# Kernel optimization log

Hardware: AMD Instinct MI355X
Metric: run time of the kernel (lower is better)

## Reference

```python
import jax, jax.numpy as jnp
import numpy as np

B, S, E, D, H = 32, 4096, 512, 512, 512


def setup_inputs() -> dict:
    key = jax.random.key(0)
    ks = jax.random.split(key, 7)
    scale = 1.0 / np.sqrt(H)
    return {
        "encoder_hiddens": jax.random.normal(ks[0], (B, S, E), dtype=jnp.float32),
        "decoder_hidden": jax.random.normal(ks[1], (B, D), dtype=jnp.float32),
        "W_enc": jax.random.uniform(ks[2], (H, E), jnp.float32, -scale, scale),
        "b_enc": jax.random.uniform(ks[3], (H,), jnp.float32, -scale, scale),
        "W_dec": jax.random.uniform(ks[4], (H, D), jnp.float32, -scale, scale),
        "b_dec": jax.random.uniform(ks[5], (H,), jnp.float32, -scale, scale),
        "v": jax.random.uniform(ks[6], (H,), jnp.float32, -scale, scale),
    }


def reference(encoder_hiddens, decoder_hidden, W_enc, b_enc, W_dec, b_dec, v):
    # Projections (the two small GEMMs of the original per-timestep loop, batched)
    enc_hs = jnp.einsum("bse,he->bsh", encoder_hiddens, W_enc) + b_enc  # [B,S,H]
    dec_h = decoder_hidden @ W_dec.T + b_dec                            # [B,H]

    # Ragged-length detection: the torch loop breaks at the first all-zero
    # projected encoder row; positions at/after that are excluded (cumulative AND).
    nonzero = jnp.any(enc_hs != 0, axis=-1)                             # [B,S]
    valid = jnp.cumprod(nonzero.astype(jnp.int32), axis=1).astype(bool)

    # Additive (Bahdanau) scores: v . tanh(enc_hs + dec_h)
    scores = jnp.einsum("h,bsh->bs", v, jnp.tanh(enc_hs + dec_h[:, None, :]))
    scores = jnp.where(valid, scores, -jnp.inf)
    attn = jax.nn.softmax(scores, axis=1)                               # [B,S]
    attn = jnp.where(valid, attn, 0.0)

    # Weighted sum of encoder states -> context vector [B,1,E]
    return jnp.sum(encoder_hiddens * attn[..., None], axis=1, keepdims=True)
```

## Files before the change

### kernel.cpp

```cpp
#include <hip/hip_runtime.h>
#include <hip/hip_bf16.h>

#define BATCH 32
#define SEQ   4096
#define EDIM  512
#define HDIM  512
#define NCHUNK 64
#define NBLK  (BATCH * NCHUNK)

typedef unsigned short u16;
typedef unsigned int   u32;

typedef __bf16 bf16x8 __attribute__((ext_vector_type(8)));
typedef float  f32x4  __attribute__((ext_vector_type(4)));

__device__ __forceinline__ u16 bf_rne(float x) {
    u32 u = __float_as_uint(x);
    u32 r = (u + 0x7fffu + ((u >> 16) & 1u)) >> 16;
    return (u16)r;
}
__device__ __forceinline__ u32 pack2(u16 lo, u16 hi) {
    return (u32)lo | ((u32)hi << 16);
}
__device__ __forceinline__ float tanh_fast(float x) {
    float e = __builtin_amdgcn_exp2f(x * 2.88539008177793f);
    return 1.0f - 2.0f * __builtin_amdgcn_rcpf(e + 1.0f);
}

__global__ void prep_kernel(const float* __restrict__ W_enc, uint4* __restrict__ wpack,
                            const float* __restrict__ dec, const float* __restrict__ Wd,
                            const float* __restrict__ b_enc, const float* __restrict__ b_dec,
                            float* __restrict__ dec_bias) {
    int bid = blockIdx.x;
    int t = threadIdx.x;
    if (bid < 4096) {
        int wave = t >> 6, lane = t & 63;
        int p = bid * 4 + wave;
        int b = p >> 9, h = p & 511;
        const float4* wr = reinterpret_cast<const float4*>(Wd)  + h * 128;
        const float4* dr = reinterpret_cast<const float4*>(dec) + b * 128;
        float4 w0 = wr[lane * 2], w1 = wr[lane * 2 + 1];
        float4 d0 = dr[lane * 2], d1 = dr[lane * 2 + 1];
        float s = w0.x * d0.x + w0.y * d0.y + w0.z * d0.z + w0.w * d0.w
                + w1.x * d1.x + w1.y * d1.y + w1.z * d1.z + w1.w * d1.w;
#pragma unroll
        for (int m = 1; m < 64; m <<= 1) s += __shfl_xor(s, m, 64);
        if (lane == 0) dec_bias[p] = s + b_dec[h] + b_enc[h];
    } else {
        int id   = (bid - 4096) * 256 + t;
        int nsub = id >> 10;
        int rem  = id & 1023;
        int kc   = rem >> 6;
        int lane = rem & 63;
        int row  = nsub * 16 + (lane & 15);
        int col  = kc * 32 + (lane >> 4) * 8;
        const float* src = W_enc + row * EDIM + col;
        uint4 o;
        o.x = pack2(bf_rne(src[0]), bf_rne(src[1]));
        o.y = pack2(bf_rne(src[2]), bf_rne(src[3]));
        o.z = pack2(bf_rne(src[4]), bf_rne(src[5]));
        o.w = pack2(bf_rne(src[6]), bf_rne(src[7]));
        wpack[id] = o;
    }
}

__global__ __launch_bounds__(256, 2) void fused_kernel(
    const float* __restrict__ X, const uint4* __restrict__ Wp,
    const float* __restrict__ bias, const float* __restrict__ v,
    float* __restrict__ cpart, float* __restrict__ mpart, float* __restrict__ lpart)
{
    __shared__ alignas(16) u16 Abuf[2][64 * 72];
    __shared__ float sred[4][64];
    __shared__ float pbuf[64];

    const int tid  = threadIdx.x;
    const int wave = tid >> 6, lane = tid & 63;
    const int quad = lane >> 4, l15 = lane & 15;
    const int blk  = blockIdx.x;
    const int b    = blk >> 6;
    const long row0 = (long)blk * 64;
    const float4* X4 = reinterpret_cast<const float4*>(X + row0 * EDIM);

    f32x4 acc[4][8] = {};

    const int r  = tid >> 2;
    const int c8 = tid & 3;

    float4 pA = X4[r * 128 + c8 * 2];
    float4 pB = X4[r * 128 + c8 * 2 + 1];
    {
        uint4 w;
        w.x = pack2(bf_rne(pA.x), bf_rne(pA.y));
        w.y = pack2(bf_rne(pA.z), bf_rne(pA.w));
        w.z = pack2(bf_rne(pB.x), bf_rne(pB.y));
        w.w = pack2(bf_rne(pB.z), bf_rne(pB.w));
        *reinterpret_cast<uint4*>(&Abuf[0][r * 72 + c8 * 8]) = w;
    }
    pA = X4[r * 128 + 8 + c8 * 2];
    pB = X4[r * 128 + 8 + c8 * 2 + 1];
    __syncthreads();

    for (int ch = 0; ch < 16; ch++) {
        const u16* Ab = Abuf[ch & 1];

        uint4 braw[8];
#pragma unroll
        for (int jj = 0; jj < 8; jj++)
            braw[jj] = Wp[((wave * 8 + jj) * 16 + ch) * 64 + lane];

        float4 nA, nB;
        if (ch < 14) {
            nA = X4[r * 128 + (ch + 2) * 8 + c8 * 2];
            nB = X4[r * 128 + (ch + 2) * 8 + c8 * 2 + 1];
        }

        bf16x8 af[4];
#pragma unroll
        for (int i = 0; i < 4; i++)
            af[i] = *reinterpret_cast<const bf16x8*>(&Ab[(i * 16 + l15) * 72 + quad * 8]);
#pragma unroll
        for (int jj = 0; jj < 8; jj++) {
            bf16x8 bfr = __builtin_bit_cast(bf16x8, braw[jj]);
#pragma unroll
            for (int i = 0; i < 4; i++)
                acc[i][jj] = __builtin_amdgcn_mfma_f32_16x16x32_bf16(
                    af[i], bfr, acc[i][jj], 0, 0, 0);
        }

        if (ch < 15) {
            uint4 w;
            w.x = pack2(bf_rne(pA.x), bf_rne(pA.y));
            w.y = pack2(bf_rne(pA.z), bf_rne(pA.w));
            w.z = pack2(bf_rne(pB.x), bf_rne(pB.y));
            w.w = pack2(bf_rne(pB.z), bf_rne(pB.w));
            *reinterpret_cast<uint4*>(&Abuf[(ch & 1) ^ 1][r * 72 + c8 * 8]) = w;
        }
        __syncthreads();
        if (ch < 14) { pA = nA; pB = nB; }
    }

    float hb[8], hv[8];
#pragma unroll
    for (int jj = 0; jj < 8; jj++) {
        int h = wave * 128 + jj * 16 + l15;
        hb[jj] = bias[b * HDIM + h];
        hv[jj] = v[h];
    }
    float s_acc[16];
#pragma unroll
    for (int x = 0; x < 16; x++) s_acc[x] = 0.f;
#pragma unroll
    for (int i = 0; i < 4; i++)
#pragma unroll
        for (int jj = 0; jj < 8; jj++)
#pragma unroll
            for (int rr = 0; rr < 4; rr++)
                s_acc[i * 4 + rr] += hv[jj] * tanh_fast(acc[i][jj][rr] + hb[jj]);

#pragma unroll
    for (int m = 1; m < 16; m <<= 1)
#pragma unroll
        for (int x = 0; x < 16; x++)
            s_acc[x] += __shfl_xor(s_acc[x], m, 16);

    if (l15 == 0) {
#pragma unroll
        for (int x = 0; x < 16; x++) {
            int i = x >> 2, rr = x & 3;
            sred[wave][i * 16 + quad * 4 + rr] = s_acc[x];
        }
    }
    __syncthreads();

    if (tid < 64) {
        float sc = sred[0][tid] + sred[1][tid] + sred[2][tid] + sred[3][tid];
        float mx = sc;
#pragma unroll
        for (int m = 1; m < 64; m <<= 1) mx = fmaxf(mx, __shfl_xor(mx, m, 64));
        float p = __builtin_amdgcn_exp2f((sc - mx) * 1.44269504088896f);
        float l = p;
#pragma unroll
        for (int m = 1; m < 64; m <<= 1) l += __shfl_xor(l, m, 64);
        pbuf[tid] = p;
        if (tid == 0) { mpart[blk] = mx; lpart[blk] = l; }
    }
    __syncthreads();

    const float2* Xp = reinterpret_cast<const float2*>(X + row0 * EDIM) + tid;
    float ax0 = 0.f, ay0 = 0.f, ax1 = 0.f, ay1 = 0.f;
#pragma unroll 2
    for (int s = 0; s < 64; s += 8) {
        float2 x[8];
#pragma unroll
        for (int k = 0; k < 8; k++) x[k] = Xp[(s + k) * 256];
#pragma unroll
        for (int k = 0; k < 8; k += 2) {
            float w0 = pbuf[s + k], w1 = pbuf[s + k + 1];
            ax0 = fmaf(w0, x[k].x,     ax0);
            ay0 = fmaf(w0, x[k].y,     ay0);
            ax1 = fmaf(w1, x[k + 1].x, ax1);
            ay1 = fmaf(w1, x[k + 1].y, ay1);
        }
    }
    reinterpret_cast<float2*>(cpart)[blk * 256 + tid] =
        make_float2(ax0 + ax1, ay0 + ay1);
}

__global__ __launch_bounds__(256) void combine_k(const float* __restrict__ cpart,
                                                 const float* __restrict__ mpart,
                                                 const float* __restrict__ lpart,
                                                 float* __restrict__ out) {
    __shared__ float wbuf[64];
    __shared__ float linv_s;
    int b = blockIdx.x, t = threadIdx.x;
    if (t < 64) {
        float m = mpart[b * 64 + t];
        float M = m;
#pragma unroll
        for (int k = 1; k < 64; k <<= 1) M = fmaxf(M, __shfl_xor(M, k, 64));
        float w = __builtin_amdgcn_exp2f((m - M) * 1.44269504088896f);
        float lw = lpart[b * 64 + t] * w;
        float L = lw;
#pragma unroll
        for (int k = 1; k < 64; k <<= 1) L += __shfl_xor(L, k, 64);
        wbuf[t] = w;
        if (t == 0) linv_s = 1.0f / L;
    }
    __syncthreads();
    const float2* cp = reinterpret_cast<const float2*>(cpart) + (long)b * 64 * 256 + t;
    float ax = 0.f, ay = 0.f;
#pragma unroll 2
    for (int i = 0; i < 64; i += 8) {
        float2 x[8];
#pragma unroll
        for (int k = 0; k < 8; k++) x[k] = cp[(i + k) * 256];
#pragma unroll
        for (int k = 0; k < 8; k++) {
            float w = wbuf[i + k];
            ax = fmaf(w, x[k].x, ax);
            ay = fmaf(w, x[k].y, ay);
        }
    }
    float inv = linv_s;
    reinterpret_cast<float2*>(out)[b * 256 + t] = make_float2(ax * inv, ay * inv);
}

extern "C" void kernel_launch(void* const* d_in, const int* in_sizes, int n_in,
                              void* d_out, int out_size, void* d_ws, size_t ws_size,
                              hipStream_t stream) {
    const float* X      = (const float*)d_in[0];
    const float* dec    = (const float*)d_in[1];
    const float* W_enc  = (const float*)d_in[2];
    const float* b_enc  = (const float*)d_in[3];
    const float* W_dec  = (const float*)d_in[4];
    const float* b_dec  = (const float*)d_in[5];
    const float* v      = (const float*)d_in[6];
    float* out = (float*)d_out;

    char* ws = (char*)d_ws;
    uint4* wpack    = (uint4*)ws;
    float* dec_bias = (float*)(ws + (512 << 10));
    float* cpart    = (float*)(ws + (576 << 10));
    float* mpart    = (float*)(ws + (576 << 10) + (4096 << 10));
    float* lpart    = (float*)(ws + (576 << 10) + (4104 << 10));

    prep_kernel  <<<4224, 256, 0, stream>>>(W_enc, wpack, dec, W_dec, b_enc, b_dec,
                                            dec_bias);
    fused_kernel <<<NBLK, 256, 0, stream>>>(X, wpack, dec_bias, v, cpart, mpart, lpart);
    combine_k    <<<BATCH, 256, 0, stream>>>(cpart, mpart, lpart, out);
}
```

Before: 447.5 us.

## Stage full bf16 X tile in LDS upfront and prefetch W fragments one chunk ahead

Replaces the double-buffered per-chunk X staging with a one-time load of the whole 64x512 X tile, converted to bf16 and held in LDS with a padded stride. This removes the per-chunk __syncthreads from the K loop. It also software-pipelines the packed W_enc fragment loads so the next chunk's loads are issued before the current MFMAs. The trade-off is a larger LDS footprint (about 66KB), which may limit occupancy, plus a serialized load phase before any compute starts.

```diff
diff --git a/kernel.cpp b/kernel.cpp
--- a/kernel.cpp
+++ b/kernel.cpp
@@ -7,6 +7,7 @@
 #define HDIM  512
 #define NCHUNK 64
 #define NBLK  (BATCH * NCHUNK)
+#define XSTRIDE 520
 
 typedef unsigned short u16;
 typedef unsigned int   u32;
@@ -69,7 +70,7 @@
     const float* __restrict__ bias, const float* __restrict__ v,
     float* __restrict__ cpart, float* __restrict__ mpart, float* __restrict__ lpart)
 {
-    __shared__ alignas(16) u16 Abuf[2][64 * 72];
+    __shared__ alignas(16) u16 Xs[64 * XSTRIDE];
     __shared__ float sred[4][64];
     __shared__ float pbuf[64];
 
@@ -81,62 +82,59 @@
     const long row0 = (long)blk * 64;
     const float4* X4 = reinterpret_cast<const float4*>(X + row0 * EDIM);
 
+    const int r  = tid >> 2;
+    const int cs = tid & 3;
+#pragma unroll
+    for (int ph = 0; ph < 2; ph++) {
+        float4 t0[8], t1[8];
+#pragma unroll
+        for (int i = 0; i < 8; i++) {
+            int ii = ph * 8 + i;
+            t0[i] = X4[r * 128 + cs * 2 + ii * 8];
+            t1[i] = X4[r * 128 + cs * 2 + ii * 8 + 1];
+        }
+#pragma unroll
+        for (int i = 0; i < 8; i++) {
+            int ii = ph * 8 + i;
+            uint4 w;
+            w.x = pack2(bf_rne(t0[i].x), bf_rne(t0[i].y));
+            w.y = pack2(bf_rne(t0[i].z), bf_rne(t0[i].w));
+            w.z = pack2(bf_rne(t1[i].x), bf_rne(t1[i].y));
+            w.w = pack2(bf_rne(t1[i].z), bf_rne(t1[i].w));
+            *reinterpret_cast<uint4*>(&Xs[r * XSTRIDE + cs * 8 + ii * 32]) = w;
+        }
+    }
+    __syncthreads();
+
     f32x4 acc[4][8] = {};
-
-    const int r  = tid >> 2;
-    const int c8 = tid & 3;
-
-    float4 pA = X4[r * 128 + c8 * 2];
-    float4 pB = X4[r * 128 + c8 * 2 + 1];
-    {
-        uint4 w;
-        w.x = pack2(bf_rne(pA.x), bf_rne(pA.y));
-        w.y = pack2(bf_rne(pA.z), bf_rne(pA.w));
-        w.z = pack2(bf_rne(pB.x), bf_rne(pB.y));
-        w.w = pack2(bf_rne(pB.z), bf_rne(pB.w));
-        *reinterpret_cast<uint4*>(&Abuf[0][r * 72 + c8 * 8]) = w;
-    }
-    pA = X4[r * 128 + 8 + c8 * 2];
-    pB = X4[r * 128 + 8 + c8 * 2 + 1];
-    __syncthreads();
-
+    uint4 bcur[8];
+#pragma unroll
+    for (int jj = 0; jj < 8; jj++)
+        bcur[jj] = Wp[((wave * 8 + jj) * 16 + 0) * 64 + lane];
+
+#pragma unroll
     for (int ch = 0; ch < 16; ch++) {
-        const u16* Ab = Abuf[ch & 1];
-
-        uint4 braw[8];
+        uint4 bnxt[8];
+        const int chn = (ch < 15) ? ch + 1 : 15;
 #pragma unroll
         for (int jj = 0; jj < 8; jj++)
-            braw[jj] = Wp[((wave * 8 + jj) * 16 + ch) * 64 + lane];
-
-        float4 nA, nB;
-        if (ch < 14) {
-            nA = X4[r * 128 + (ch + 2) * 8 + c8 * 2];
-            nB = X4[r * 128 + (ch + 2) * 8 + c8 * 2 + 1];
-        }
+            bnxt[jj] = Wp[((wave * 8 + jj) * 16 + chn) * 64 + lane];
 
         bf16x8 af[4];
 #pragma unroll
         for (int i = 0; i < 4; i++)
-            af[i] = *reinterpret_cast<const bf16x8*>(&Ab[(i * 16 + l15) * 72 + quad * 8]);
+            af[i] = *reinterpret_cast<const bf16x8*>(
+                &Xs[(i * 16 + l15) * XSTRIDE + ch * 32 + quad * 8]);
 #pragma unroll
         for (int jj = 0; jj < 8; jj++) {
-            bf16x8 bfr = __builtin_bit_cast(bf16x8, braw[jj]);
+            bf16x8 bfr = __builtin_bit_cast(bf16x8, bcur[jj]);
 #pragma unroll
             for (int i = 0; i < 4; i++)
                 acc[i][jj] = __builtin_amdgcn_mfma_f32_16x16x32_bf16(
                     af[i], bfr, acc[i][jj], 0, 0, 0);
         }
-
-        if (ch < 15) {
-            uint4 w;
-            w.x = pack2(bf_rne(pA.x), bf_rne(pA.y));
-            w.y = pack2(bf_rne(pA.z), bf_rne(pA.w));
-            w.z = pack2(bf_rne(pB.x), bf_rne(pB.y));
-            w.w = pack2(bf_rne(pB.z), bf_rne(pB.w));
-            *reinterpret_cast<uint4*>(&Abuf[(ch & 1) ^ 1][r * 72 + c8 * 8]) = w;
-        }
-        __syncthreads();
-        if (ch < 14) { pA = nA; pB = nB; }
+#pragma unroll
+        for (int jj = 0; jj < 8; jj++) bcur[jj] = bnxt[jj];
     }
 
     float hb[8], hv[8];
```

Result: slower. 531.2 us (+18.7%).
